# Kernel tuning notes

Measured on AMD Instinct MI355X. Metric: run time of the kernel, lower is better.

## Reference

```python
import jax, jax.numpy as jnp
import numpy as np

N_NODES = 50000
N_EDGES = 800000
NFEAT = 64
HID = 64
NCLASS = 10


def setup_inputs() -> dict:
    key = jax.random.key(0)
    ks = jax.random.split(key, 12)
    x = jax.random.normal(ks[0], (N_NODES, NFEAT), dtype=jnp.float32)
    edge_index = jax.random.randint(ks[1], (2, N_EDGES), 0, N_NODES, dtype=jnp.int64)
    edge_attr = jax.random.uniform(ks[2], (N_EDGES,), dtype=jnp.float32)
    # GCNConv layer params (glorot-ish scale)
    W1 = jax.random.normal(ks[3], (NFEAT, HID), dtype=jnp.float32) / np.sqrt(NFEAT)
    b1 = jnp.zeros((HID,), dtype=jnp.float32)
    W2 = jax.random.normal(ks[4], (HID, HID), dtype=jnp.float32) / np.sqrt(HID)
    b2 = jnp.zeros((HID,), dtype=jnp.float32)
    fc1_w = jax.random.normal(ks[5], (HID, 128), dtype=jnp.float32) / np.sqrt(HID)
    fc1_b = jnp.zeros((128,), dtype=jnp.float32)
    fc2_w = jax.random.normal(ks[6], (128, NCLASS), dtype=jnp.float32) / np.sqrt(128.0)
    fc2_b = jnp.zeros((NCLASS,), dtype=jnp.float32)
    return {"x": x, "edge_index": edge_index, "edge_attr": edge_attr,
            "W1": W1, "b1": b1, "W2": W2, "b2": b2,
            "fc1_w": fc1_w, "fc1_b": fc1_b, "fc2_w": fc2_w, "fc2_b": fc2_b}


def reference(x, edge_index, edge_attr, W1, b1, W2, b2, fc1_w, fc1_b, fc2_w, fc2_b):
    N = x.shape[0]
    # add_self_loops: append (i, i) edges; self-loop edge weight = 1
    loops = jnp.arange(N, dtype=edge_index.dtype)
    row = jnp.concatenate([edge_index[0], loops])
    col = jnp.concatenate([edge_index[1], loops])
    ew = jnp.concatenate([edge_attr, jnp.ones((N,), dtype=x.dtype)])
    # symmetric degree normalization: deg = degree(row); D^{-1/2} A D^{-1/2}
    deg = jax.ops.segment_sum(jnp.ones_like(ew), row, num_segments=N)
    dis = deg ** -0.5  # deg >= 1 due to self loops
    norm_w = dis[row] * ew * dis[col]  # [E+N]

    def gcn_conv(h, W, b):
        h = h @ W                                    # [N, d_out]
        msg = norm_w[:, None] * h[col]               # [E+N, d_out] gather
        agg = jax.ops.segment_sum(msg, row, num_segments=N)  # scatter-add
        return agg + b

    h = jax.nn.relu(gcn_conv(x, W1, b1))  # dropout is identity in eval mode
    h = gcn_conv(h, W2, b2)               # no activation after last conv
    h = jax.nn.relu(h @ fc1_w + fc1_b)
    return h @ fc2_w + fc2_b
```

## Files before the change

### kernel.cpp

```cpp
#include <hip/hip_runtime.h>


#define NFEAT 64
#define PAD 64


__global__ void k_fill(const int* __restrict__ row, const int* __restrict__ col,
                       const float* __restrict__ ew, int* __restrict__ cur,
                       int2* __restrict__ csr, int ne, int npb) {
    int xcd = blockIdx.x & 7;
    int bid = blockIdx.x >> 3;
    int nbg = gridDim.x >> 3;
    int i0 = bid * blockDim.x + threadIdx.x;
    int stride = nbg * blockDim.x;
#pragma unroll
    for (int sub = 0; sub < 2; ++sub) {
        int bucket = xcd * 2 + sub;
        int lo = bucket * npb;
        int hi = lo + npb;
        for (int i = i0; i < ne; i += stride) {
            int r = row[i];
            if (r >= lo && r < hi) {
                int slot = atomicAdd(&cur[r], 1);
                if (slot < PAD)
                    csr[((size_t)r << 6) + slot] =
                        make_int2(col[i], __float_as_int(ew[i]));
            }
        }
    }
}


__global__ __launch_bounds__(256, 4) void k_gemm_dis(const float* __restrict__ x,
                                                     const float* __restrict__ W1,
                                                     const int* __restrict__ cur,
                                                     float* __restrict__ dis,
                                                     float* __restrict__ H, int N) {
    __shared__ float XT[64 * 68];
    __shared__ float Wl[64 * 64];
    int tid = threadIdx.x;
    int r0 = blockIdx.x * 64;
    if (tid < 64) {
        int i = r0 + tid;
        if (i < N) dis[i] = rsqrtf(1.0f + (float)cur[i]);
    }
    for (int i = tid; i < 64 * 64; i += 256) Wl[i] = W1[i];
    for (int i = tid; i < 64 * 64; i += 256) {
        int r = i >> 6, k = i & 63;
        int rr = r0 + r;
        XT[k * 68 + r] = (rr < N) ? x[(size_t)r0 * 64 + i] : 0.f;
    }
    __syncthreads();
    int f4 = (tid & 15) * 4;
    int r4 = (tid >> 4) * 4;
    float acc[4][4];
#pragma unroll
    for (int i = 0; i < 4; ++i)
#pragma unroll
        for (int j = 0; j < 4; ++j) acc[i][j] = 0.f;
#pragma unroll 8
    for (int k = 0; k < 64; ++k) {
        float4 w = *(const float4*)&Wl[k * 64 + f4];
        float4 xv = *(const float4*)&XT[k * 68 + r4];
        float xs[4] = {xv.x, xv.y, xv.z, xv.w};
        float ws[4] = {w.x, w.y, w.z, w.w};
#pragma unroll
        for (int i = 0; i < 4; ++i)
#pragma unroll
            for (int j = 0; j < 4; ++j) acc[i][j] = fmaf(xs[i], ws[j], acc[i][j]);
    }
#pragma unroll
    for (int i = 0; i < 4; ++i) {
        int rr = r0 + r4 + i;
        if (rr < N) {
            float4 o = make_float4(acc[i][0], acc[i][1], acc[i][2], acc[i][3]);
            *(float4*)&H[(size_t)rr * 64 + f4] = o;
        }
    }
}


__device__ __forceinline__ float4 agg_row(const int* cur, const float* dis,
                                          const int2* csr, const float* H,
                                          int node, int sub, int q4) {
    int cnt = cur[node];
    int ce = cnt > PAD ? PAD : cnt;
    size_t base = (size_t)node << 6;
    float4 acc = make_float4(0.f, 0.f, 0.f, 0.f);
    int e = sub;
    for (; e + 4 < ce; e += 8) {
        int2 p0 = csr[base + e];
        int2 p1 = csr[base + e + 4];
        float w0 = __int_as_float(p0.y) * dis[p0.x];
        float w1 = __int_as_float(p1.y) * dis[p1.x];
        float4 h0 = *(const float4*)&H[(size_t)p0.x * 64 + q4];
        float4 h1 = *(const float4*)&H[(size_t)p1.x * 64 + q4];
        acc.x = fmaf(w0, h0.x, acc.x);
        acc.y = fmaf(w0, h0.y, acc.y);
        acc.z = fmaf(w0, h0.z, acc.z);
        acc.w = fmaf(w0, h0.w, acc.w);
        acc.x = fmaf(w1, h1.x, acc.x);
        acc.y = fmaf(w1, h1.y, acc.y);
        acc.z = fmaf(w1, h1.z, acc.z);
        acc.w = fmaf(w1, h1.w, acc.w);
    }
    if (e < ce) {
        int2 p = csr[base + e];
        float w = __int_as_float(p.y) * dis[p.x];
        float4 h = *(const float4*)&H[(size_t)p.x * 64 + q4];
        acc.x = fmaf(w, h.x, acc.x);
        acc.y = fmaf(w, h.y, acc.y);
        acc.z = fmaf(w, h.z, acc.z);
        acc.w = fmaf(w, h.w, acc.w);
    }
#pragma unroll
    for (int m = 16; m <= 32; m <<= 1) {
        acc.x += __shfl_xor(acc.x, m, 64);
        acc.y += __shfl_xor(acc.y, m, 64);
        acc.z += __shfl_xor(acc.z, m, 64);
        acc.w += __shfl_xor(acc.w, m, 64);
    }
    return acc;
}


__global__ __launch_bounds__(256) void k_agg(const int* __restrict__ cur,
                                             const float* __restrict__ dis,
                                             const int2* __restrict__ csr,
                                             const float* __restrict__ H,
                                             float* __restrict__ AGG, int n) {
    int l = threadIdx.x & 63;
    int node = (blockIdx.x * blockDim.x + threadIdx.x) >> 6;
    if (node >= n) return;
    int sub = l >> 4;
    int q4 = (l & 15) * 4;
    float4 acc = agg_row(cur, dis, csr, H, node, sub, q4);
    if (sub == 0) {
        float d = dis[node];
        float4 hs = *(const float4*)&H[(size_t)node * 64 + q4];
        float4 o;
        o.x = fmaf(d, hs.x, acc.x) * d;
        o.y = fmaf(d, hs.y, acc.y) * d;
        o.z = fmaf(d, hs.z, acc.z) * d;
        o.w = fmaf(d, hs.w, acc.w) * d;
        *(float4*)&AGG[(size_t)node * 64 + q4] = o;
    }
}


__global__ __launch_bounds__(256) void k_agg_fused(const int* __restrict__ cur,
                                                   const float* __restrict__ dis,
                                                   const int2* __restrict__ csr,
                                                   const float* __restrict__ H1,
                                                   const float* __restrict__ b1,
                                                   const float* __restrict__ W2,
                                                   float* __restrict__ H2, int n) {
    __shared__ float W2l[64 * 64];
    __shared__ float pbuf[4][64];
    int tid = threadIdx.x;
    for (int i = tid; i < 64 * 64; i += 256) W2l[i] = W2[i];
    __syncthreads();
    int l = tid & 63;
    int wv = tid >> 6;
    int sub = l >> 4;
    int q4 = (l & 15) * 4;
    int nwaves = (gridDim.x * blockDim.x) >> 6;
    for (int node = (blockIdx.x * blockDim.x + tid) >> 6; node < n; node += nwaves) {
        float4 acc = agg_row(cur, dis, csr, H1, node, sub, q4);
        float d = dis[node];
        float4 hs = *(const float4*)&H1[(size_t)node * 64 + q4];
        float4 bq = *(const float4*)&b1[q4];
        float4 p;
        p.x = fmaxf(fmaf(d, hs.x, acc.x) * d + bq.x, 0.f);
        p.y = fmaxf(fmaf(d, hs.y, acc.y) * d + bq.y, 0.f);
        p.z = fmaxf(fmaf(d, hs.z, acc.z) * d + bq.z, 0.f);
        p.w = fmaxf(fmaf(d, hs.w, acc.w) * d + bq.w, 0.f);
        if (sub == 0) *(float4*)&pbuf[wv][q4] = p;
        asm volatile("" ::: "memory");
        float sum = 0.f;
#pragma unroll
        for (int q = 0; q < 16; ++q) {
            float4 v = *(const float4*)&pbuf[wv][q * 4];
            sum = fmaf(v.x, W2l[(q * 4 + 0) * 64 + l], sum);
            sum = fmaf(v.y, W2l[(q * 4 + 1) * 64 + l], sum);
            sum = fmaf(v.z, W2l[(q * 4 + 2) * 64 + l], sum);
            sum = fmaf(v.w, W2l[(q * 4 + 3) * 64 + l], sum);
        }
        asm volatile("" ::: "memory");
        H2[(size_t)node * 64 + l] = sum;
    }
}


__global__ __launch_bounds__(256, 4) void k_mlp(const float* __restrict__ AGG,
                                                const float* __restrict__ b2,
                                                const float* __restrict__ fc1w,
                                                const float* __restrict__ fc1b,
                                                const float* __restrict__ fc2w,
                                                const float* __restrict__ fc2b,
                                                float* __restrict__ out, int n) {
    __shared__ float XT[64 * 68];
    __shared__ float Wh[64 * 64];
    __shared__ float W2l[128 * 10];
    __shared__ float b1l[128];
    __shared__ float b2c[16];
    int tid = threadIdx.x;
    int r0 = blockIdx.x * 64;
    for (int i = tid; i < 64 * 64; i += 256) {
        int r = i >> 6, k = i & 63;
        int rr = r0 + r;
        float v = 0.f;
        if (rr < n) v = AGG[(size_t)r0 * 64 + i] + b2[k];
        XT[k * 68 + r] = v;
    }
    for (int i = tid; i < 64 * 64; i += 256)
        Wh[i] = fc1w[(i >> 6) * 128 + (i & 63)];
    for (int i = tid; i < 128 * 10; i += 256) W2l[i] = fc2w[i];
    if (tid < 128) b1l[tid] = fc1b[tid];
    if (tid < 10) b2c[tid] = fc2b[tid];
    float wreg[16];
#pragma unroll
    for (int i = 0; i < 16; ++i) {
        int idx = i * 256 + tid;
        wreg[i] = fc1w[(idx >> 6) * 128 + 64 + (idx & 63)];
    }
    __syncthreads();

    int f4 = (tid & 15) * 4;
    int r4 = (tid >> 4) * 4;
    float pacc[4][10];
#pragma unroll
    for (int i = 0; i < 4; ++i)
#pragma unroll
        for (int c = 0; c < 10; ++c) pacc[i][c] = 0.f;

#pragma unroll
    for (int h = 0; h < 2; ++h) {
        if (h == 1) {
            __syncthreads();
#pragma unroll
            for (int i = 0; i < 16; ++i) Wh[i * 256 + tid] = wreg[i];
            __syncthreads();
        }
        float acc[4][4];
#pragma unroll
        for (int i = 0; i < 4; ++i)
#pragma unroll
            for (int j = 0; j < 4; ++j) acc[i][j] = 0.f;
#pragma unroll 8
        for (int k = 0; k < 64; ++k) {
            float4 xv = *(const float4*)&XT[k * 68 + r4];
            float4 wv = *(const float4*)&Wh[k * 64 + f4];
            float xs[4] = {xv.x, xv.y, xv.z, xv.w};
            float ws[4] = {wv.x, wv.y, wv.z, wv.w};
#pragma unroll
            for (int i = 0; i < 4; ++i)
#pragma unroll
                for (int j = 0; j < 4; ++j) acc[i][j] = fmaf(xs[i], ws[j], acc[i][j]);
        }
#pragma unroll
        for (int jj = 0; jj < 4; ++jj) {
            int jcol = h * 64 + f4 + jj;
            float w2r[10];
#pragma unroll
            for (int c = 0; c < 10; ++c) w2r[c] = W2l[jcol * 10 + c];
            float bj = b1l[jcol];
#pragma unroll
            for (int i = 0; i < 4; ++i) {
                float pv = fmaxf(acc[i][jj] + bj, 0.f);
#pragma unroll
                for (int c = 0; c < 10; ++c) pacc[i][c] = fmaf(pv, w2r[c], pacc[i][c]);
            }
        }
    }
#pragma unroll
    for (int i = 0; i < 4; ++i)
#pragma unroll
        for (int c = 0; c < 10; ++c) {
            float v = pacc[i][c];
            v += __shfl_xor(v, 1, 64);
            v += __shfl_xor(v, 2, 64);
            v += __shfl_xor(v, 4, 64);
            v += __shfl_xor(v, 8, 64);
            pacc[i][c] = v;
        }
    if ((tid & 15) == 0) {
#pragma unroll
        for (int i = 0; i < 4; ++i) {
            int rr = r0 + r4 + i;
            if (rr < n) {
#pragma unroll
                for (int c = 0; c < 10; ++c)
                    out[(size_t)rr * 10 + c] = pacc[i][c] + b2c[c];
            }
        }
    }
}


extern "C" void kernel_launch(void* const* d_in, const int* in_sizes, int n_in,
                              void* d_out, int out_size, void* d_ws, size_t ws_size,
                              hipStream_t stream) {
    const float* x     = (const float*)d_in[0];
    const int*   eidx  = (const int*)d_in[1];
    const float* eattr = (const float*)d_in[2];
    const float* W1    = (const float*)d_in[3];
    const float* b1    = (const float*)d_in[4];
    const float* W2    = (const float*)d_in[5];
    const float* b2    = (const float*)d_in[6];
    const float* fc1w  = (const float*)d_in[7];
    const float* fc1b  = (const float*)d_in[8];
    const float* fc2w  = (const float*)d_in[9];
    const float* fc2b  = (const float*)d_in[10];
    float* out = (float*)d_out;

    int N = in_sizes[0] / NFEAT;
    int E = in_sizes[2];
    const int* row = eidx;
    const int* col = eidx + E;

    int*   cur  = (int*)d_ws;
    float* dis  = (float*)(cur + 50176);
    int2*  csr  = (int2*)(dis + 50176);
    float* H    = (float*)(csr + (size_t)50176 * 64);
    float* H2   = H + (size_t)N * 64;

    const int TB = 256;
    int gG = (N + 63) / 64;
    int gA = (N * 64 + TB - 1) / TB;
    int npb = (N + 15) / 16;

    hipMemsetAsync(cur, 0, (size_t)N * sizeof(int), stream);
    k_fill<<<2048, TB, 0, stream>>>(row, col, eattr, cur, csr, E, npb);
    k_gemm_dis<<<gG, TB, 0, stream>>>(x, W1, cur, dis, H, N);
    k_agg_fused<<<2048, TB, 0, stream>>>(cur, dis, csr, H, b1, W2, H2, N);
    k_agg<<<gA, TB, 0, stream>>>(cur, dis, csr, H2, H, N);
    k_mlp<<<gG, TB, 0, stream>>>(H, b2, fc1w, fc1b, fc2w, fc2b, out, N);
}
```

Baseline: 243.1 us.

## Replace repeated edge filtering with two-pass binning before CSR scatter

```diff
diff --git a/kernel.cpp b/kernel.cpp
--- a/kernel.cpp
+++ b/kernel.cpp
@@ -3,28 +3,50 @@
 
 #define NFEAT 64
 #define PAD 64
-
-
-__global__ void k_fill(const int* __restrict__ row, const int* __restrict__ col,
-                       const float* __restrict__ ew, int* __restrict__ cur,
-                       int2* __restrict__ csr, int ne, int npb) {
+#define NBUCK 16
+#define NPB 3136
+#define LCAP 10000
+
+
+__global__ void k_bin(const int* __restrict__ row, const int* __restrict__ col,
+                      const float* __restrict__ ew, int* __restrict__ bcur,
+                      int4* __restrict__ lists, int ne) {
     int xcd = blockIdx.x & 7;
+    int i = blockIdx.x * blockDim.x + threadIdx.x;
+    int stride = gridDim.x * blockDim.x;
+    for (; i < ne; i += stride) {
+        int r = row[i];
+        int tb = r / NPB;
+        int li = xcd * NBUCK + tb;
+        int pos = atomicAdd(&bcur[li], 1);
+        if (pos < LCAP)
+            lists[(size_t)li * LCAP + pos] =
+                make_int4(r, col[i], __float_as_int(ew[i]), 0);
+    }
+}
+
+
+__global__ void k_scatter2(const int* __restrict__ bcur,
+                           const int4* __restrict__ lists,
+                           int* __restrict__ cur, int2* __restrict__ csr) {
+    int g = blockIdx.x & 7;
     int bid = blockIdx.x >> 3;
     int nbg = gridDim.x >> 3;
-    int i0 = bid * blockDim.x + threadIdx.x;
-    int stride = nbg * blockDim.x;
+    int tstride = nbg * blockDim.x;
+    int t0 = bid * blockDim.x + threadIdx.x;
 #pragma unroll
     for (int sub = 0; sub < 2; ++sub) {
-        int bucket = xcd * 2 + sub;
-        int lo = bucket * npb;
-        int hi = lo + npb;
-        for (int i = i0; i < ne; i += stride) {
-            int r = row[i];
-            if (r >= lo && r < hi) {
-                int slot = atomicAdd(&cur[r], 1);
+        int tb = g * 2 + sub;
+#pragma unroll
+        for (int w = 0; w < 8; ++w) {
+            int li = w * NBUCK + tb;
+            int cnt = bcur[li];
+            if (cnt > LCAP) cnt = LCAP;
+            for (int i = t0; i < cnt; i += tstride) {
+                int4 en = lists[(size_t)li * LCAP + i];
+                int slot = atomicAdd(&cur[en.x], 1);
                 if (slot < PAD)
-                    csr[((size_t)r << 6) + slot] =
-                        make_int2(col[i], __float_as_int(ew[i]));
+                    csr[((size_t)en.x << 6) + slot] = make_int2(en.y, en.z);
             }
         }
     }
@@ -319,19 +341,21 @@
     const int* row = eidx;
     const int* col = eidx + E;
 
-    int*   cur  = (int*)d_ws;
-    float* dis  = (float*)(cur + 50176);
-    int2*  csr  = (int2*)(dis + 50176);
-    float* H    = (float*)(csr + (size_t)50176 * 64);
-    float* H2   = H + (size_t)N * 64;
+    int*   cur   = (int*)d_ws;
+    int*   bcur  = cur + 50176;
+    float* dis   = (float*)(bcur + 256);
+    int4*  lists = (int4*)(dis + 50176);
+    int2*  csr   = (int2*)(lists + (size_t)128 * LCAP);
+    float* H     = (float*)(csr + (size_t)50176 * 64);
+    float* H2    = H + (size_t)N * 64;
 
     const int TB = 256;
     int gG = (N + 63) / 64;
     int gA = (N * 64 + TB - 1) / TB;
-    int npb = (N + 15) / 16;
-
-    hipMemsetAsync(cur, 0, (size_t)N * sizeof(int), stream);
-    k_fill<<<2048, TB, 0, stream>>>(row, col, eattr, cur, csr, E, npb);
+
+    hipMemsetAsync(cur, 0, (size_t)(50176 + 256) * sizeof(int), stream);
+    k_bin<<<2048, TB, 0, stream>>>(row, col, eattr, bcur, lists, E);
+    k_scatter2<<<2048, TB, 0, stream>>>(bcur, lists, cur, csr);
     k_gemm_dis<<<gG, TB, 0, stream>>>(x, W1, cur, dis, H, N);
     k_agg_fused<<<2048, TB, 0, stream>>>(cur, dis, csr, H, b1, W2, H2, N);
     k_agg<<<gA, TB, 0, stream>>>(cur, dis, csr, H2, H, N);
```

Measured after the change: 695.5 us. 2.86x slower.
